# Optimization experiments

Hardware: AMD Instinct MI355X
Metric: run time of the kernel (lower is better)

## Reference

```python
import jax, jax.numpy as jnp
import numpy as np

N = 262144        # number of 3D coordinate points (64^3 grid, flattened)
LW = 64           # layer_width
NOISE_DIM = 16
C_DIM = 3
NODES = 12        # 1 input node + 11 hidden graph nodes

# Frozen random-graph topology: predecessors of hidden node i (node 0 is the input node).
PREDS = ((0,), (1,), (2, 0), (3, 1, 0), (4, 2), (5, 3), (6, 4), (7, 5, 0), (8, 6), (9, 7), (10, 8))

def gauss(t):
    return jnp.exp(-0.5 * t * t)

# 'basic' activation set, cycled through graph nodes
ACTS = (jnp.tanh, jax.nn.elu, jax.nn.softplus, jnp.sin, gauss, jax.nn.sigmoid)


def setup_inputs() -> dict:
    key = jax.random.key(0)
    ks = jax.random.split(key, 16)
    n_g = NODES - 1
    inp = {
        "x": jax.random.normal(ks[0], (N, 1), jnp.float32),
        "y": jax.random.normal(ks[1], (N, 1), jnp.float32),
        "z": jax.random.normal(ks[2], (N, 1), jnp.float32),
        "r": jax.random.normal(ks[3], (N, 1), jnp.float32),
        "noise": jax.random.normal(ks[4], (N, NOISE_DIM), jnp.float32),
        # learned parameters
        "W_noise": jax.random.normal(ks[5], (NOISE_DIM, LW), jnp.float32) / np.sqrt(NOISE_DIM),
        "b_noise": jnp.zeros((LW,), jnp.float32),
        "W_x": jax.random.normal(ks[6], (1, LW), jnp.float32),
        "W_y": jax.random.normal(ks[7], (1, LW), jnp.float32),
        "W_z": jax.random.normal(ks[8], (1, LW), jnp.float32),
        "W_r": jax.random.normal(ks[9], (1, LW), jnp.float32),
        "W1": jax.random.normal(ks[10], (LW, LW), jnp.float32) / np.sqrt(LW),
        "b1": jnp.zeros((LW,), jnp.float32),
        "Wg": jax.random.normal(ks[11], (n_g, LW, LW), jnp.float32) / np.sqrt(LW),
        "bg": jnp.zeros((n_g, LW), jnp.float32),
        "W_out": jax.random.normal(ks[12], (LW, C_DIM), jnp.float32) / np.sqrt(LW),
        "b_out": jnp.zeros((C_DIM,), jnp.float32),
    }
    return inp


def reference(x, y, z, r, noise, W_noise, b_noise, W_x, W_y, W_z, W_r, W1, b1, Wg, bg, W_out, b_out):
    # input branches: tiny dim-1 linears + distinct pointwise activations
    noise_ = jnp.tanh(noise @ W_noise + b_noise)   # [N, LW]
    z_ = jax.nn.elu(z @ W_z)
    r_ = jax.nn.softplus(r @ W_r)
    y_ = jnp.tanh(y @ W_y)
    x_ = gauss(x @ W_x)
    f = jnp.sin(z_ + x_ + y_ + r_ + noise_)
    f = jnp.tanh(f @ W1 + b1)
    # randomly-wired graph of small linear+activation nodes (frozen topology)
    h = [f]
    for i, preds in enumerate(PREDS):
        s = h[preds[0]]
        for p in preds[1:]:
            s = s + h[p]
        h.append(ACTS[i % len(ACTS)](s @ Wg[i] + bg[i]))
    out = h[-1] @ W_out + b_out                    # combine node -> c_dim
    return jax.nn.sigmoid(out)                     # act_out (clip_loss=False)
```

## Files before the change

### kernel.cpp

```cpp
#include <hip/hip_runtime.h>

typedef _Float16 f16;
typedef f16  f16x4 __attribute__((ext_vector_type(4)));
typedef f16  f16x8 __attribute__((ext_vector_type(8)));
typedef float f32x2  __attribute__((ext_vector_type(2)));
typedef float f32x4  __attribute__((ext_vector_type(4)));
typedef float f32x16 __attribute__((ext_vector_type(16)));
typedef unsigned int u32;
typedef u32 u32x2 __attribute__((ext_vector_type(2)));
typedef u32 u32x4 __attribute__((ext_vector_type(4)));

#define LOG2E   1.4426950408889634f
#define LN2     0.6931471805599453f
#define C_TANH  2.8853900817779268f
#define C_SIN   0.15915494309189535f
#define C_SIG  -1.4426950408889634f
#define C_GAU  -0.7213475204444817f
#define C_GSQ   0.84932180028802f

__device__ __constant__ float NSCL[12] = {
    C_TANH, C_TANH, 1.0f, LOG2E, C_SIN, C_GSQ, C_SIG, C_TANH, 1.0f, LOG2E, C_SIN, C_GSQ
};

__device__ __forceinline__ float frcp(float x){ return __builtin_amdgcn_rcpf(x); }
__device__ __forceinline__ float fexp2(float x){ return __builtin_amdgcn_exp2f(x); }
__device__ __forceinline__ float flog2(float x){ return __builtin_amdgcn_logf(x); }
__device__ __forceinline__ float fsin1(float x){ return __builtin_amdgcn_sinf(x); }

template<int A> __device__ __forceinline__ f32x2 act2(f32x2 v){
    if constexpr (A == 0){
        f32x2 t = {fexp2(v.x), fexp2(v.y)};
        f32x2 u = t + 1.0f;
        f32x2 rc = {frcp(u.x), frcp(u.y)};
        return rc * -2.0f + 1.0f;
    } else if constexpr (A == 1){
        f32x2 w = v * LOG2E;
        f32x2 e = {fexp2(w.x), fexp2(w.y)};
        f32x2 em1 = e - 1.0f;
        f32x2 z = {0.0f, 0.0f};
        return __builtin_elementwise_max(v, z) + __builtin_elementwise_min(em1, z);
    } else if constexpr (A == 2){
        f32x2 e = {fexp2(v.x), fexp2(v.y)};
        f32x2 u = e + 1.0f;
        f32x2 l = {flog2(u.x), flog2(u.y)};
        return l * LN2;
    } else if constexpr (A == 3){
        return f32x2{fsin1(v.x), fsin1(v.y)};
    } else if constexpr (A == 4){
        f32x2 w = -(v * v);
        return f32x2{fexp2(w.x), fexp2(w.y)};
    } else {
        f32x2 e = {fexp2(v.x), fexp2(v.y)};
        f32x2 u = e + 1.0f;
        return f32x2{frcp(u.x), frcp(u.y)};
    }
}

__device__ __forceinline__ f16x4 pack4(float a, float b, float c, float d){
    u32x2 u;
    u[0] = __builtin_bit_cast(u32, __builtin_amdgcn_cvt_pkrtz(a, b));
    u[1] = __builtin_bit_cast(u32, __builtin_amdgcn_cvt_pkrtz(c, d));
    return __builtin_bit_cast(f16x4, u);
}
__device__ __forceinline__ f16x8 cat8(f16x4 lo, f16x4 hi){
    u32x2 a = __builtin_bit_cast(u32x2, lo), b = __builtin_bit_cast(u32x2, hi);
    u32x4 u; u[0] = a[0]; u[1] = a[1]; u[2] = b[0]; u[3] = b[1];
    return __builtin_bit_cast(f16x8, u);
}

#define MFMA32(a, b, c) __builtin_amdgcn_mfma_f32_32x32x16_f16((a), (b), (c), 0, 0, 0)

template<int ACTI, int NP>
__device__ __forceinline__ void node32(const f16* __restrict__ wr,
                                       const float* __restrict__ bs,
                                       const int hf4,
                                       const f16x8 A0[4], const f16x8 A1[4], const f16x8 A2[4],
                                       f16x8 OUT[4])
{
    f16x4 pk[2][4];
    #pragma unroll
    for (int t = 0; t < 2; ++t){
        f32x16 a;
        #pragma unroll
        for (int g = 0; g < 4; ++g){
            f32x4 bv = *(const f32x4*)(bs + 32 * t + 8 * g + hf4);
            a[4*g+0] = bv[0]; a[4*g+1] = bv[1]; a[4*g+2] = bv[2]; a[4*g+3] = bv[3];
        }
        #pragma unroll
        for (int kc = 0; kc < 4; ++kc){
            f16x8 Af = *(const f16x8*)(wr + t * 2048 + kc * 512);
            f16x8 bB = A0[kc];
            if constexpr (NP >= 2){ bB = bB + A1[kc]; }
            if constexpr (NP >= 3){ bB = bB + A2[kc]; }
            a = MFMA32(Af, bB, a);
        }
        #pragma unroll
        for (int g = 0; g < 4; ++g){
            f32x2 v01 = {a[4*g+0], a[4*g+1]};
            f32x2 v23 = {a[4*g+2], a[4*g+3]};
            f32x2 o01 = act2<ACTI>(v01);
            f32x2 o23 = act2<ACTI>(v23);
            pk[t][g] = pack4(o01.x, o01.y, o23.x, o23.y);
        }
    }
    #pragma unroll
    for (int kc = 0; kc < 4; ++kc)
        OUT[kc] = cat8(pk[0][kc], pk[1][kc]);
}

__global__ __launch_bounds__(1024, 1) void inr_mfma8_kernel(
    const float* __restrict__ gx, const float* __restrict__ gy,
    const float* __restrict__ gz, const float* __restrict__ gr,
    const float* __restrict__ gnoise,
    const float* __restrict__ W_noise, const float* __restrict__ b_noise,
    const float* __restrict__ W_x, const float* __restrict__ W_y,
    const float* __restrict__ W_z, const float* __restrict__ W_r,
    const float* __restrict__ W1, const float* __restrict__ b1,
    const float* __restrict__ Wg, const float* __restrict__ bg,
    const float* __restrict__ W_out, const float* __restrict__ b_out,
    float* __restrict__ out, int nt, int niter)
{
    __shared__ __align__(16) f16   wfrag[12][2][4][64][8];
    __shared__ __align__(16) f16   nfrag[2][64][8];
    __shared__ __align__(16) f16   ofrag[4][64][8];
    __shared__ __align__(16) float b_s[12][64];
    __shared__ __align__(16) float wvs[4][64];
    __shared__ __align__(16) float bns[64];
    __shared__            float bout_s[4];

    const int tid  = threadIdx.x;
    const int lane = tid & 63;
    const int n2   = lane & 31;
    const int hf   = lane >> 5;
    const int hf4  = 4 * hf;

    if (tid < 768){
        int node = tid >> 6, f = tid & 63;
        b_s[node][f] = NSCL[node] * ((node == 0) ? b1[f] : bg[(node - 1) * 64 + f]);
    }
    if (tid < 256){
        int vec = tid >> 6, f = tid & 63;
        float v;
        if      (vec == 0){ float w = W_x[f]; v = C_GAU * w * w; }
        else if (vec == 1){ v = C_TANH * W_y[f]; }
        else if (vec == 2){ v = W_z[f]; }
        else              { v = LOG2E * W_r[f]; }
        wvs[vec][f] = v;
    }
    if (tid < 64) bns[tid] = C_TANH * b_noise[tid];
    if (tid < 4)  bout_s[tid] = (tid < 3) ? C_SIG * b_out[tid] : 0.0f;
    if (tid < 128){
        int t = tid >> 6, ln = tid & 63, m = ln & 31, h = ln >> 5;
        f16x8 v;
        #pragma unroll
        for (int j = 0; j < 8; ++j) v[j] = (f16)(C_TANH * W_noise[(8 * h + j) * 64 + 32 * t + m]);
        *(f16x8*)&nfrag[t][ln][0] = v;
    }
    if (tid < 256){
        int kc = tid >> 6, ln = tid & 63, m = ln & 31, h = ln >> 5;
        f16x8 v;
        #pragma unroll
        for (int j = 0; j < 8; ++j){
            int kf = 8 * kc + 32 * (j >> 2) + 4 * h + (j & 3);
            v[j] = (m < 3) ? (f16)(C_SIG * W_out[kf * 3 + m]) : (f16)0.0f;
        }
        *(f16x8*)&ofrag[kc][ln][0] = v;
    }
    {
        const int sub = tid & 511;
        const int t = sub >> 8, kc = (sub >> 6) & 3, ln = sub & 63, m = ln & 31, h = ln >> 5;
        int kfo[8];
        #pragma unroll
        for (int j = 0; j < 8; ++j)
            kfo[j] = (8 * kc + 32 * (j >> 2) + 4 * h + (j & 3)) * 64 + 32 * t + m;
        #pragma unroll
        for (int node = tid >> 9; node < 12; node += 2){
            const float* Wsrc = (node == 0) ? W1 : (Wg + (node - 1) * 4096);
            const float  scl  = NSCL[node];
            f16x8 v;
            #pragma unroll
            for (int j = 0; j < 8; ++j) v[j] = (f16)(scl * Wsrc[kfo[j]]);
            *(f16x8*)&wfrag[node][t][kc][ln][0] = v;
        }
    }
    __syncthreads();

    #define WPTR(NI) (&wfrag[NI][0][0][lane][0])
    #define N1(NI, ACTI, A, OUT)        node32<ACTI,1>(WPTR(NI), &b_s[NI][0], hf4, A, A, A, OUT)
    #define N2(NI, ACTI, A, B, OUT)     node32<ACTI,2>(WPTR(NI), &b_s[NI][0], hf4, A, B, B, OUT)
    #define N3(NI, ACTI, A, B, C, OUT)  node32<ACTI,3>(WPTR(NI), &b_s[NI][0], hf4, A, B, C, OUT)

    const int wvid = tid >> 6;

    for (int it = 0; it < niter; ++it){
        const int tile = (it * gridDim.x + blockIdx.x) * 16 + wvid;
        if (tile >= nt) break;
        const int myp = tile * 32 + n2;

        f16x8 ra[4];
        {
            const float xs = gx[myp], ys = gy[myp], zs = gz[myp], rs = gr[myp];
            const float xs2 = xs * xs;
            f16x8 nb;
            {
                const float4 a4 = *(const float4*)(gnoise + (size_t)myp * 16 + 8 * hf);
                const float4 b4 = *(const float4*)(gnoise + (size_t)myp * 16 + 8 * hf + 4);
                nb = cat8(pack4(a4.x, a4.y, a4.z, a4.w), pack4(b4.x, b4.y, b4.z, b4.w));
            }
            f16x4 pkg[2][4];
            #pragma unroll
            for (int t = 0; t < 2; ++t){
                f32x16 ac;
                #pragma unroll
                for (int i = 0; i < 16; ++i) ac[i] = 0.0f;
                ac = MFMA32(*(const f16x8*)&nfrag[t][lane][0], nb, ac);
                #pragma unroll
                for (int g = 0; g < 4; ++g){
                    const int fb = 32 * t + 8 * g + hf4;
                    const f32x4 wx2 = *(const f32x4*)&wvs[0][fb];
                    const f32x4 wyt = *(const f32x4*)&wvs[1][fb];
                    const f32x4 wz  = *(const f32x4*)&wvs[2][fb];
                    const f32x4 wr_ = *(const f32x4*)&wvs[3][fb];
                    const f32x4 bn  = *(const f32x4*)&bns[fb];
                    f32x2 sv[2];
                    #pragma unroll
                    for (int p = 0; p < 2; ++p){
                        const f32x2 z2 = {0.0f, 0.0f};
                        f32x2 wzp = {wz[2*p], wz[2*p+1]};
                        f32x2 az  = zs * wzp;
                        f32x2 we  = az * LOG2E;
                        f32x2 ee  = {fexp2(we.x), fexp2(we.y)};
                        f32x2 em1 = ee - 1.0f;
                        f32x2 el  = __builtin_elementwise_max(az, z2)
                                  + __builtin_elementwise_min(em1, z2);
                        f32x2 wxp = {wx2[2*p], wx2[2*p+1]};
                        f32x2 wg  = xs2 * wxp;
                        f32x2 ga  = {fexp2(wg.x), fexp2(wg.y)};
                        f32x2 wyp = {wyt[2*p], wyt[2*p+1]};
                        f32x2 wy  = ys * wyp;
                        f32x2 tty = {fexp2(wy.x), fexp2(wy.y)};
                        f32x2 uy  = tty + 1.0f;
                        f32x2 ry  = {frcp(uy.x), frcp(uy.y)};
                        f32x2 ty  = ry * -2.0f + 1.0f;
                        f32x2 wrp = {wr_[2*p], wr_[2*p+1]};
                        f32x2 wsp = rs * wrp;
                        f32x2 es  = {fexp2(wsp.x), fexp2(wsp.y)};
                        f32x2 us  = es + 1.0f;
                        f32x2 ls  = {flog2(us.x), flog2(us.y)};
                        f32x2 sp  = ls * LN2;
                        f32x2 acp = {ac[4*g+2*p], ac[4*g+2*p+1]};
                        f32x2 bnp = {bn[2*p], bn[2*p+1]};
                        f32x2 wt  = acp + bnp;
                        f32x2 ttp = {fexp2(wt.x), fexp2(wt.y)};
                        f32x2 up  = ttp + 1.0f;
                        f32x2 rp  = {frcp(up.x), frcp(up.y)};
                        f32x2 tp  = rp * -2.0f + 1.0f;
                        sv[p] = ((el + ga) + (ty + sp) + tp) * C_SIN;
                    }
                    pkg[t][g] = pack4(fsin1(sv[0].x), fsin1(sv[0].y),
                                      fsin1(sv[1].x), fsin1(sv[1].y));
                }
            }
            #pragma unroll
            for (int kc = 0; kc < 4; ++kc) ra[kc] = cat8(pkg[0][kc], pkg[1][kc]);
        }

        f16x8 h0[4], rb[4], rc[4], rd[4];
        N1(0,  0, ra, h0);
        N1(1,  0, h0, ra);
        N1(2,  1, ra, rb);
        N2(3,  2, rb, h0, rc);
        N3(4,  3, rc, ra, h0, rd);
        N2(5,  4, rd, rb, ra);
        N2(6,  5, ra, rc, rb);
        N2(7,  0, rb, rd, rc);
        N3(8,  1, rc, ra, h0, rd);
        N2(9,  2, rd, rb, ra);
        N2(10, 3, ra, rc, rb);
        N2(11, 4, rb, rd, rc);

        {
            f32x16 om;
            #pragma unroll
            for (int i = 0; i < 16; ++i) om[i] = 0.0f;
            #pragma unroll
            for (int kc = 0; kc < 4; ++kc)
                om = MFMA32(*(const f16x8*)&ofrag[kc][lane][0], rc[kc], om);
            if (hf == 0){
                #pragma unroll
                for (int r = 0; r < 3; ++r)
                    out[(size_t)myp * 3 + r] = frcp(1.0f + fexp2(om[r] + bout_s[r]));
            }
        }
    }
    #undef N1
    #undef N2
    #undef N3
    #undef WPTR
}

extern "C" void kernel_launch(void* const* d_in, const int* in_sizes, int n_in,
                              void* d_out, int out_size, void* d_ws, size_t ws_size,
                              hipStream_t stream)
{
    const float* x       = (const float*)d_in[0];
    const float* y       = (const float*)d_in[1];
    const float* z       = (const float*)d_in[2];
    const float* r       = (const float*)d_in[3];
    const float* noise   = (const float*)d_in[4];
    const float* W_noise = (const float*)d_in[5];
    const float* b_noise = (const float*)d_in[6];
    const float* W_x     = (const float*)d_in[7];
    const float* W_y     = (const float*)d_in[8];
    const float* W_z     = (const float*)d_in[9];
    const float* W_r     = (const float*)d_in[10];
    const float* W1      = (const float*)d_in[11];
    const float* b1      = (const float*)d_in[12];
    const float* Wg      = (const float*)d_in[13];
    const float* bg      = (const float*)d_in[14];
    const float* W_out   = (const float*)d_in[15];
    const float* b_out   = (const float*)d_in[16];
    float* out = (float*)d_out;

    const int n     = in_sizes[0];
    const int nt    = n / 32;
    const int grid  = 256;
    const int tiles_per_pass = grid * 16;
    const int niter = (nt + tiles_per_pass - 1) / tiles_per_pass;
    inr_mfma8_kernel<<<dim3(grid), dim3(1024), 0, stream>>>(
        x, y, z, r, noise, W_noise, b_noise, W_x, W_y, W_z, W_r,
        W1, b1, Wg, bg, W_out, b_out, out, nt, niter);
}
```

Measured before the change: 152.2 us.

## Interleave the two output-half MFMA chains and remap the K fragment layout

Each graph node now runs the two 32-column MFMA accumulator chains interleaved rather than one after the other. Independent MFMAs can then overlap in the pipeline instead of waiting on a single dependent chain. The K-fragment packing of activations is changed so each output half maps to contiguous K chunks. The weight and W_out fragment index maps are updated to match. Interleaving raises register pressure because two f32x16 accumulators are live at once.

```diff
diff --git a/kernel.cpp b/kernel.cpp
--- a/kernel.cpp
+++ b/kernel.cpp
@@ -77,35 +77,41 @@
                                        const f16x8 A0[4], const f16x8 A1[4], const f16x8 A2[4],
                                        f16x8 OUT[4])
 {
-    f16x4 pk[2][4];
+    f32x16 a0, a1;
     #pragma unroll
-    for (int t = 0; t < 2; ++t){
-        f32x16 a;
-        #pragma unroll
-        for (int g = 0; g < 4; ++g){
-            f32x4 bv = *(const f32x4*)(bs + 32 * t + 8 * g + hf4);
-            a[4*g+0] = bv[0]; a[4*g+1] = bv[1]; a[4*g+2] = bv[2]; a[4*g+3] = bv[3];
-        }
-        #pragma unroll
-        for (int kc = 0; kc < 4; ++kc){
-            f16x8 Af = *(const f16x8*)(wr + t * 2048 + kc * 512);
-            f16x8 bB = A0[kc];
-            if constexpr (NP >= 2){ bB = bB + A1[kc]; }
-            if constexpr (NP >= 3){ bB = bB + A2[kc]; }
-            a = MFMA32(Af, bB, a);
-        }
-        #pragma unroll
-        for (int g = 0; g < 4; ++g){
-            f32x2 v01 = {a[4*g+0], a[4*g+1]};
-            f32x2 v23 = {a[4*g+2], a[4*g+3]};
-            f32x2 o01 = act2<ACTI>(v01);
-            f32x2 o23 = act2<ACTI>(v23);
-            pk[t][g] = pack4(o01.x, o01.y, o23.x, o23.y);
-        }
+    for (int g = 0; g < 4; ++g){
+        f32x4 b0 = *(const f32x4*)(bs +      8 * g + hf4);
+        f32x4 b1 = *(const f32x4*)(bs + 32 + 8 * g + hf4);
+        a0[4*g+0] = b0[0]; a0[4*g+1] = b0[1]; a0[4*g+2] = b0[2]; a0[4*g+3] = b0[3];
+        a1[4*g+0] = b1[0]; a1[4*g+1] = b1[1]; a1[4*g+2] = b1[2]; a1[4*g+3] = b1[3];
     }
     #pragma unroll
-    for (int kc = 0; kc < 4; ++kc)
-        OUT[kc] = cat8(pk[0][kc], pk[1][kc]);
+    for (int kc = 0; kc < 4; ++kc){
+        f16x8 bB = A0[kc];
+        if constexpr (NP >= 2){ bB = bB + A1[kc]; }
+        if constexpr (NP >= 3){ bB = bB + A2[kc]; }
+        const f16x8 W0 = *(const f16x8*)(wr +        kc * 512);
+        const f16x8 W1 = *(const f16x8*)(wr + 2048 + kc * 512);
+        a0 = MFMA32(W0, bB, a0);
+        a1 = MFMA32(W1, bB, a1);
+    }
+    f16x4 pk0[4], pk1[4];
+    #pragma unroll
+    for (int g = 0; g < 4; ++g){
+        f32x2 o01 = act2<ACTI>(f32x2{a0[4*g+0], a0[4*g+1]});
+        f32x2 o23 = act2<ACTI>(f32x2{a0[4*g+2], a0[4*g+3]});
+        pk0[g] = pack4(o01.x, o01.y, o23.x, o23.y);
+    }
+    OUT[0] = cat8(pk0[0], pk0[1]);
+    OUT[1] = cat8(pk0[2], pk0[3]);
+    #pragma unroll
+    for (int g = 0; g < 4; ++g){
+        f32x2 o01 = act2<ACTI>(f32x2{a1[4*g+0], a1[4*g+1]});
+        f32x2 o23 = act2<ACTI>(f32x2{a1[4*g+2], a1[4*g+3]});
+        pk1[g] = pack4(o01.x, o01.y, o23.x, o23.y);
+    }
+    OUT[2] = cat8(pk1[0], pk1[1]);
+    OUT[3] = cat8(pk1[2], pk1[3]);
 }
 
 __global__ __launch_bounds__(1024, 1) void inr_mfma8_kernel(
@@ -161,7 +167,7 @@
         f16x8 v;
         #pragma unroll
         for (int j = 0; j < 8; ++j){
-            int kf = 8 * kc + 32 * (j >> 2) + 4 * h + (j & 3);
+            int kf = 16 * kc + 8 * (j >> 2) + 4 * h + (j & 3);
             v[j] = (m < 3) ? (f16)(C_SIG * W_out[kf * 3 + m]) : (f16)0.0f;
         }
         *(f16x8*)&ofrag[kc][ln][0] = v;
@@ -172,7 +178,7 @@
         int kfo[8];
         #pragma unroll
         for (int j = 0; j < 8; ++j)
-            kfo[j] = (8 * kc + 32 * (j >> 2) + 4 * h + (j & 3)) * 64 + 32 * t + m;
+            kfo[j] = (16 * kc + 8 * (j >> 2) + 4 * h + (j & 3)) * 64 + 32 * t + m;
         #pragma unroll
         for (int node = tid >> 9; node < 12; node += 2){
             const float* Wsrc = (node == 0) ? W1 : (Wg + (node - 1) * 4096);
@@ -207,13 +213,15 @@
                 const float4 b4 = *(const float4*)(gnoise + (size_t)myp * 16 + 8 * hf + 4);
                 nb = cat8(pack4(a4.x, a4.y, a4.z, a4.w), pack4(b4.x, b4.y, b4.z, b4.w));
             }
+            f32x16 ac0, ac1;
+            #pragma unroll
+            for (int i = 0; i < 16; ++i){ ac0[i] = 0.0f; ac1[i] = 0.0f; }
+            ac0 = MFMA32(*(const f16x8*)&nfrag[0][lane][0], nb, ac0);
+            ac1 = MFMA32(*(const f16x8*)&nfrag[1][lane][0], nb, ac1);
             f16x4 pkg[2][4];
             #pragma unroll
             for (int t = 0; t < 2; ++t){
-                f32x16 ac;
-                #pragma unroll
-                for (int i = 0; i < 16; ++i) ac[i] = 0.0f;
-                ac = MFMA32(*(const f16x8*)&nfrag[t][lane][0], nb, ac);
+                const f32x16& ac = t ? ac1 : ac0;
                 #pragma unroll
                 for (int g = 0; g < 4; ++g){
                     const int fb = 32 * t + 8 * g + hf4;
@@ -261,8 +269,10 @@
                                       fsin1(sv[1].x), fsin1(sv[1].y));
                 }
             }
-            #pragma unroll
-            for (int kc = 0; kc < 4; ++kc) ra[kc] = cat8(pkg[0][kc], pkg[1][kc]);
+            ra[0] = cat8(pkg[0][0], pkg[0][1]);
+            ra[1] = cat8(pkg[0][2], pkg[0][3]);
+            ra[2] = cat8(pkg[1][0], pkg[1][1]);
+            ra[3] = cat8(pkg[1][2], pkg[1][3]);
         }
 
         f16x8 h0[4], rb[4], rc[4], rd[4];
```

Result: no change. 153.6 us (+0.9%).
